# Kernel tuning notes

Hardware: AMD Instinct MI355X
Metric: run time of the kernel (lower is better)

## Reference

```python
import jax, jax.numpy as jnp
import numpy as np

N = 100000
E = 1600000
R = 8
DIN = 128
H = 128
C = 16
NROOT = 1024


def rgcn_conv(x, src, dst, edge_type, w_rel, w_root, bias):
    """PyG RGCNConv: per-relation mean aggregation + root weight + bias."""
    n, din = x.shape
    r = w_rel.shape[0]
    msgs = x[src]  # [E, din] gather
    seg = dst * r + edge_type  # combined (node, relation) segment id
    sums = jax.ops.segment_sum(msgs, seg, num_segments=n * r)        # [N*R, din]
    cnt = jax.ops.segment_sum(jnp.ones((msgs.shape[0],), x.dtype), seg,
                              num_segments=n * r)                    # [N*R]
    mean = sums / jnp.maximum(cnt, 1.0)[:, None]
    mean = mean.reshape(n, r, din)
    # relation-specific transform then sum over relations, plus root transform
    out = jnp.einsum('nrd,rde->ne', mean, w_rel) + x @ w_root + bias
    return out


def setup_inputs() -> dict:
    key = jax.random.key(0)
    ks = jax.random.split(key, 16)
    s = 0.05
    return {
        'x': jax.random.normal(ks[0], (N, DIN), jnp.float32),
        'edge_index': jax.random.randint(ks[1], (2, E), 0, N, jnp.int64),
        'edge_type': jax.random.randint(ks[2], (E,), 0, R, jnp.int64),
        'root_idx': jax.random.randint(ks[3], (NROOT,), 0, N, jnp.int64),
        'wrel1': jax.random.normal(ks[4], (R, DIN, H), jnp.float32) * s,
        'root1': jax.random.normal(ks[5], (DIN, H), jnp.float32) * s,
        'b1': jax.random.normal(ks[6], (H,), jnp.float32) * s,
        'wrel2': jax.random.normal(ks[7], (R, H, H), jnp.float32) * s,
        'root2': jax.random.normal(ks[8], (H, H), jnp.float32) * s,
        'b2': jax.random.normal(ks[9], (H,), jnp.float32) * s,
        'wrel3': jax.random.normal(ks[10], (R, H, C), jnp.float32) * s,
        'root3': jax.random.normal(ks[11], (H, C), jnp.float32) * s,
        'b3': jax.random.normal(ks[12], (C,), jnp.float32) * s,
    }


def reference(x, edge_index, edge_type, root_idx,
              wrel1, root1, b1, wrel2, root2, b2, wrel3, root3, b3):
    src, dst = edge_index[0], edge_index[1]
    h = jax.nn.relu(rgcn_conv(x, src, dst, edge_type, wrel1, root1, b1))
    # hidden conv (relu; dropout is identity in eval mode)
    h = jax.nn.relu(rgcn_conv(h, src, dst, edge_type, wrel2, root2, b2))
    # final conv, no activation
    h = rgcn_conv(h, src, dst, edge_type, wrel3, root3, b3)
    return h[root_idx]  # [NROOT, C]
```

## Files before the change

### kernel.cpp

```cpp
#include <hip/hip_runtime.h>
#include <hip/hip_fp16.h>


typedef _Float16 f16;
typedef _Float16 f16x2 __attribute__((ext_vector_type(2)));
typedef _Float16 f16x4 __attribute__((ext_vector_type(4)));
typedef _Float16 f16x8 __attribute__((ext_vector_type(8)));
typedef float f32x4 __attribute__((ext_vector_type(4)));

#define NREL 8
#define ACHUNK 8192
#define WTELEM (640 * 128)

__global__ void k_hist(const int* __restrict__ dst, int E, int* __restrict__ cnt) {
  int e = blockIdx.x * 256 + threadIdx.x;
  if (e < E) atomicAdd(&cnt[dst[e]], 1);
}

__global__ void k_scan1(const int* __restrict__ in, int* __restrict__ out,
                        int* __restrict__ part, int n) {
  __shared__ int sh[256];
  int b = blockIdx.x, t = threadIdx.x;
  int base = b * 4096 + t * 16;
  int v[16]; int s = 0;
#pragma unroll
  for (int j = 0; j < 16; j++) { int idx = base + j; int x = (idx < n) ? in[idx] : 0; v[j] = s; s += x; }
  sh[t] = s; __syncthreads();
  for (int off = 1; off < 256; off <<= 1) {
    int x = 0; if (t >= off) x = sh[t - off];
    __syncthreads();
    if (t >= off) sh[t] += x;
    __syncthreads();
  }
  int excl = (t == 0) ? 0 : sh[t - 1];
  if (t == 255) part[b] = sh[255];
#pragma unroll
  for (int j = 0; j < 16; j++) { int idx = base + j; if (idx < n) out[idx] = v[j] + excl; }
}

__global__ void k_scan2(int* __restrict__ part, int nb) {
  __shared__ int sh[256];
  int t = threadIdx.x;
  sh[t] = (t < nb) ? part[t] : 0; __syncthreads();
  for (int off = 1; off < 256; off <<= 1) {
    int x = 0; if (t >= off) x = sh[t - off];
    __syncthreads();
    if (t >= off) sh[t] += x;
    __syncthreads();
  }
  if (t < nb) part[t] = (t == 0) ? 0 : sh[t - 1];
}

__global__ void k_scan3(int* __restrict__ out, const int* __restrict__ part, int n) {
  int i = blockIdx.x * 256 + threadIdx.x;
  if (i < n) out[i] += part[i >> 12];
}

__global__ void k_scatter(const int* __restrict__ src, const int* __restrict__ dstv,
                          const int* __restrict__ et, int E,
                          const int* __restrict__ off, int* __restrict__ fill,
                          int* __restrict__ sps) {
  int e = blockIdx.x * 256 + threadIdx.x;
  if (e >= E) return;
  int d = dstv[e];
  int pos = off[d] + atomicAdd(&fill[d], 1);
  sps[pos] = src[e] | (et[e] << 20);
}

__global__ __launch_bounds__(256) void k_sinvp(const int* __restrict__ sps,
                                               const int* __restrict__ off,
                                               float* __restrict__ sinvp, int N) {
  __shared__ int c[16][8];
  int t = threadIdx.x;
  int g = t >> 4, st = t & 15;
  int n = blockIdx.x * 16 + g;
  if (st < 8) c[g][st] = 0;
  __syncthreads();
  if (n < N) {
    int e0 = off[n], e1 = off[n + 1];
    for (int e = e0 + st; e < e1; e += 16)
      atomicAdd(&c[g][((unsigned)sps[e]) >> 20], 1);
  }
  __syncthreads();
  if (n < N && st < 8) {
    int cc = c[g][st];
    sinvp[n * 8 + st] = 1.0f / (float)(cc > 1 ? cc : 1);
  }
}

__global__ void k_sentinel(int* __restrict__ p, int v) { *p = v; }

__global__ __launch_bounds__(256) void k_bhist(const int* __restrict__ dstv, int E,
                                               int* __restrict__ bcnt, int nbuck) {
  __shared__ int h[512];
  int t = threadIdx.x;
  for (int i = t; i < 512; i += 256) h[i] = 0;
  __syncthreads();
  int lo = blockIdx.x * ACHUNK;
  int hi = lo + ACHUNK < E ? lo + ACHUNK : E;
  for (int e = lo + t; e < hi; e += 256) atomicAdd(&h[dstv[e] >> 8], 1);
  __syncthreads();
  for (int i = t; i < nbuck; i += 256)
    if (h[i]) atomicAdd(&bcnt[i], h[i]);
}

__global__ __launch_bounds__(512) void k_bscan(const int* __restrict__ bcnt,
                                               int* __restrict__ boff, int nbuck) {
  __shared__ int sh[512];
  int t = threadIdx.x;
  sh[t] = (t < nbuck) ? bcnt[t] : 0;
  __syncthreads();
  for (int o = 1; o < 512; o <<= 1) {
    int v = 0; if (t >= o) v = sh[t - o];
    __syncthreads();
    sh[t] += v;
    __syncthreads();
  }
  if (t <= nbuck && t < 512) boff[t] = (t == 0) ? 0 : sh[t - 1];
  if (t == 511 && nbuck >= 512) boff[nbuck] = sh[511];
}

__global__ __launch_bounds__(256) void k_bucketA(
    const int* __restrict__ src, const int* __restrict__ dstv,
    const int* __restrict__ et, int E, const int* __restrict__ boff,
    int* __restrict__ bfill, int* __restrict__ tmp, int nbuck) {
  __shared__ int hist[512];
  __shared__ int base[512];
  int t = threadIdx.x;
  int lo = blockIdx.x * ACHUNK;
  int hi = lo + ACHUNK < E ? lo + ACHUNK : E;
  for (int i = t; i < nbuck; i += 256) hist[i] = 0;
  __syncthreads();
  for (int e = lo + t; e < hi; e += 256)
    atomicAdd(&hist[dstv[e] >> 8], 1);
  __syncthreads();
  for (int i = t; i < nbuck; i += 256) {
    int c = hist[i];
    base[i] = c ? (boff[i] + atomicAdd(&bfill[i], c)) : 0;
  }
  __syncthreads();
  for (int e = lo + t; e < hi; e += 256) {
    int d = dstv[e];
    int b = d >> 8;
    int pos = atomicAdd(&base[b], 1);
    tmp[pos] = src[e] | (et[e] << 20) | ((d & 255) << 23);
  }
}

__global__ __launch_bounds__(256) void k_bucketB3(const int* __restrict__ tmp,
                                                  const int* __restrict__ boff,
                                                  int* __restrict__ off,
                                                  int* __restrict__ sps,
                                                  float* __restrict__ sinvp, int N) {
  __shared__ int cty[2048];
  __shared__ int sh[256];
  __shared__ int loff[257];
  __shared__ int fill[256];
  int b = blockIdx.x, t = threadIdx.x;
  int n0 = b << 8;
  int nn = (N - n0) < 256 ? (N - n0) : 256;
#pragma unroll
  for (int j = 0; j < 8; j++) cty[t + j * 256] = 0;
  __syncthreads();
  int e0 = boff[b], e1 = boff[b + 1];
  for (int e = e0 + t; e < e1; e += 256) {
    int v = tmp[e];
    int dl = (v >> 23) & 255, ty = (v >> 20) & 7;
    atomicAdd(&cty[dl * 8 + ty], 1);
  }
  __syncthreads();
  {
    int c = 0;
#pragma unroll
    for (int j = 0; j < 8; j++) c += cty[t * 8 + j];
    sh[t] = c;
  }
  __syncthreads();
  for (int o = 1; o < 256; o <<= 1) {
    int v = 0; if (t >= o) v = sh[t - o];
    __syncthreads();
    sh[t] += v;
    __syncthreads();
  }
  loff[t] = (t == 0) ? 0 : sh[t - 1];
  if (t == 255) loff[256] = sh[255];
  __syncthreads();
  if (t < nn) off[n0 + t] = e0 + loff[t];
  for (int i = t; i < 2048; i += 256) {
    int n = n0 + (i >> 3);
    if (n < N) {
      int c = cty[i];
      sinvp[(size_t)n * 8 + (i & 7)] = 1.0f / (float)(c > 1 ? c : 1);
    }
  }
  fill[t] = 0;
  __syncthreads();
  for (int e = e0 + t; e < e1; e += 256) {
    int v = tmp[e];
    int dl = (v >> 23) & 255;
    int pos = e0 + loff[dl] + atomicAdd(&fill[dl], 1);
    sps[pos] = v & 0x7FFFFF;
  }
}

__global__ void k_mark(const int* __restrict__ ridx, const int* __restrict__ off,
                       const int* __restrict__ sps, int* __restrict__ mark) {
  int i = blockIdx.x, t = threadIdx.x;
  int n = ridx[i];
  if (t == 0) mark[n] = 1;
  int e0 = off[n], e1 = off[n + 1];
  for (int e = e0 + t; e < e1; e += 64) mark[sps[e] & 0xFFFFF] = 1;
}

__global__ void k_compact(const int* __restrict__ mark, int* __restrict__ midx,
                          int* __restrict__ mlist, int* __restrict__ nm, int N) {
  int n = blockIdx.x * 256 + threadIdx.x;
  if (n < N && mark[n]) {
    int i = atomicAdd(nm, 1);
    midx[n] = i;
    mlist[i] = n;
  }
}

__global__ void k_tpw4(const float* __restrict__ wrel1, const float* __restrict__ root1,
                       f16* __restrict__ Wt, int PW) {
  int row = blockIdx.x, k = threadIdx.x, q = blockIdx.y;
  float v = 0.f;
  if (row < 9 * PW) {
    int cb = row / PW, j = row - cb * PW;
    int col = q * PW + j;
    v = (cb < 8) ? wrel1[(size_t)cb * 16384 + k * 128 + col] : root1[k * 128 + col];
  }
  Wt[(size_t)q * WTELEM + (size_t)row * 128 + k] = (f16)v;
}

__global__ void k_tpwc2(const float* __restrict__ wrel2, const float* __restrict__ root2,
                        f16* __restrict__ Wc) {
  int c = blockIdx.x, k = threadIdx.x;
#pragma unroll
  for (int r = 0; r < 8; r++)
    Wc[(size_t)c * 1152 + r * 128 + k] = (f16)wrel2[(size_t)r * 16384 + k * 128 + c];
  Wc[(size_t)c * 1152 + 1024 + k] = (f16)root2[(size_t)k * 128 + c];
}

template <typename AT>
__global__ __launch_bounds__(256) void k_gemm3(const AT* __restrict__ A,
                                               const f16* __restrict__ Bt,
                                               f16* __restrict__ Y, int M, int ncol) {
  __shared__ f16 As[128 * 136];
  int tid = threadIdx.x;
  int m0 = blockIdx.x * 128;
  int PW = ncol / 9;
  int cbs = (PW == 64) ? 6 : 5;
#pragma unroll
  for (int cch = 0; cch < 8; cch++) {
    int ci = tid + cch * 256;
    int row = ci >> 4, c8 = ci & 15;
    int gm = m0 + row;
    f16x8 va = {};
    if (gm < M) {
      if constexpr (sizeof(AT) == 2) {
        va = *(const f16x8*)((const f16*)A + (size_t)gm * 128 + c8 * 8);
      } else {
        const float4* ap = (const float4*)((const float*)A + (size_t)gm * 128);
        float4 u0 = ap[c8 * 2], u1 = ap[c8 * 2 + 1];
        va[0] = (f16)u0.x; va[1] = (f16)u0.y; va[2] = (f16)u0.z; va[3] = (f16)u0.w;
        va[4] = (f16)u1.x; va[5] = (f16)u1.y; va[6] = (f16)u1.z; va[7] = (f16)u1.w;
      }
    }
    *(f16x8*)(As + row * 136 + c8 * 8) = va;
  }
  __syncthreads();
  int wid = tid >> 6, lane = tid & 63;
  int wm = (wid & 1) * 64, wn = (wid >> 1) * 64;
  int lm = lane & 15, lk = lane >> 4;
  f16x8 af[4][4];
#pragma unroll
  for (int ks = 0; ks < 4; ks++)
#pragma unroll
    for (int i = 0; i < 4; i++)
      af[ks][i] = *(const f16x8*)(As + (wm + i * 16 + lm) * 136 + ks * 32 + lk * 8);
  __syncthreads();
  f16* H = As;
  int NT = (ncol + 127) >> 7;
  for (int nt = blockIdx.y; nt < NT; nt += gridDim.y) {
    int n0 = nt * 128;
    f32x4 acc[4][4] = {};
#pragma unroll
    for (int ks = 0; ks < 4; ks++) {
      f16x8 b[4];
#pragma unroll
      for (int j = 0; j < 4; j++)
        b[j] = *(const f16x8*)(Bt + (size_t)(n0 + wn + j * 16 + lm) * 128 + ks * 32 + lk * 8);
#pragma unroll
      for (int i = 0; i < 4; i++)
#pragma unroll
        for (int j = 0; j < 4; j++)
          acc[i][j] = __builtin_amdgcn_mfma_f32_16x16x32_f16(b[j], af[ks][i], acc[i][j], 0, 0, 0);
    }
#pragma unroll
    for (int i = 0; i < 4; i++)
#pragma unroll
      for (int j = 0; j < 4; j++) {
        f16x4 o;
        o[0] = (f16)acc[i][j][0]; o[1] = (f16)acc[i][j][1];
        o[2] = (f16)acc[i][j][2]; o[3] = (f16)acc[i][j][3];
        *(f16x4*)(H + (wm + i * 16 + lm) * 136 + wn + j * 16 + lk * 4) = o;
      }
    __syncthreads();
    for (int i = tid; i < 128 * 16; i += 256) {
      int row = i >> 4, c8 = i & 15;
      int gm = m0 + row;
      int gc = n0 + c8 * 8;
      if (gm < M && gc < ncol) {
        int cb = gc >> cbs, wi = gc & (PW - 1);
        *(f16x8*)(Y + ((size_t)cb * M + gm) * PW + wi) =
            *(const f16x8*)(H + row * 136 + c8 * 8);
      }
    }
    __syncthreads();
  }
}

template <int PW>
__global__ __launch_bounds__(256) void k_edge_v(
    const f16* __restrict__ Y, const int* __restrict__ sps,
    const int* __restrict__ off, const float* __restrict__ sinvp,
    const float* __restrict__ bias, f16* __restrict__ hout, int N, int pass) {
  constexpr int CPL = PW / 16;
  int t = threadIdx.x;
  int g = t >> 4, st = t & 15;
  int n = blockIdx.x * 16 + g;
  if (n >= N) return;
  float sv = (st < 8) ? sinvp[n * 8 + st] : 0.f;
  int e0 = off[n], e1 = off[n + 1];
  float a[CPL], b2[CPL];
  {
    const f16* rp = Y + ((size_t)8 * N + n) * PW + st * CPL;
    const float* bp = bias + pass * PW + st * CPL;
#pragma unroll
    for (int q = 0; q < CPL; q++) { a[q] = (float)rp[q] + bp[q]; b2[q] = 0.f; }
  }
  int sgbase = t & 48;
  int e = e0;
  for (; e + 1 < e1; e += 2) {
    int p0 = sps[e], p1 = sps[e + 1];
    int s0 = p0 & 0xFFFFF, ty0 = ((unsigned)p0) >> 20;
    int s1 = p1 & 0xFFFFF, ty1 = ((unsigned)p1) >> 20;
    float sc0 = __shfl(sv, sgbase | ty0);
    float sc1 = __shfl(sv, sgbase | ty1);
    const f16* q0 = Y + ((size_t)ty0 * N + s0) * PW + st * CPL;
    const f16* q1 = Y + ((size_t)ty1 * N + s1) * PW + st * CPL;
    if constexpr (PW == 64) {
      f16x4 v0 = *(const f16x4*)q0;
      f16x4 v1 = *(const f16x4*)q1;
      a[0] += (float)v0[0] * sc0; a[1] += (float)v0[1] * sc0;
      a[2] += (float)v0[2] * sc0; a[3] += (float)v0[3] * sc0;
      b2[0] += (float)v1[0] * sc1; b2[1] += (float)v1[1] * sc1;
      b2[2] += (float)v1[2] * sc1; b2[3] += (float)v1[3] * sc1;
    } else {
      f16x2 v0 = *(const f16x2*)q0;
      f16x2 v1 = *(const f16x2*)q1;
      a[0] += (float)v0[0] * sc0; a[1] += (float)v0[1] * sc0;
      b2[0] += (float)v1[0] * sc1; b2[1] += (float)v1[1] * sc1;
    }
  }
  if (e < e1) {
    int p0 = sps[e];
    int s0 = p0 & 0xFFFFF, ty0 = ((unsigned)p0) >> 20;
    float sc0 = __shfl(sv, sgbase | ty0);
    const f16* q0 = Y + ((size_t)ty0 * N + s0) * PW + st * CPL;
    if constexpr (PW == 64) {
      f16x4 v0 = *(const f16x4*)q0;
      a[0] += (float)v0[0] * sc0; a[1] += (float)v0[1] * sc0;
      a[2] += (float)v0[2] * sc0; a[3] += (float)v0[3] * sc0;
    } else {
      f16x2 v0 = *(const f16x2*)q0;
      a[0] += (float)v0[0] * sc0; a[1] += (float)v0[1] * sc0;
    }
  }
  if constexpr (PW == 64) {
    f16x4 o;
#pragma unroll
    for (int q = 0; q < 4; q++) o[q] = (f16)fmaxf(a[q] + b2[q], 0.f);
    *(f16x4*)(hout + (size_t)n * 128 + pass * PW + st * 4) = o;
  } else {
    f16x2 o;
#pragma unroll
    for (int q = 0; q < 2; q++) o[q] = (f16)fmaxf(a[q] + b2[q], 0.f);
    *(f16x2*)(hout + (size_t)n * 128 + pass * PW + st * 2) = o;
  }
}

__global__ __launch_bounds__(128) void k_agg2(
    const f16* __restrict__ h1, const int* __restrict__ sps,
    const int* __restrict__ off, const float* __restrict__ sinvp,
    const int* __restrict__ mlist, const int* __restrict__ nm_p,
    f16* __restrict__ Mc, int cap) {
  int nm = *nm_p; if (nm > cap) nm = cap;
  int t = threadIdx.x;
  for (int i = blockIdx.x; i < nm; i += gridDim.x) {
    int n = mlist[i];
    int e0 = off[n], e1 = off[n + 1];
    float acc[8];
#pragma unroll
    for (int r = 0; r < 8; r++) acc[r] = 0.f;
    int e = e0;
    for (; e + 1 < e1; e += 2) {
      int p0 = sps[e], p1 = sps[e + 1];
      int s0 = p0 & 0xFFFFF, ty0 = ((unsigned)p0) >> 20;
      int s1 = p1 & 0xFFFFF, ty1 = ((unsigned)p1) >> 20;
      float v0 = (float)h1[(size_t)s0 * 128 + t];
      float v1 = (float)h1[(size_t)s1 * 128 + t];
#pragma unroll
      for (int r = 0; r < 8; r++) {
        acc[r] += (ty0 == r) ? v0 : 0.f;
        acc[r] += (ty1 == r) ? v1 : 0.f;
      }
    }
    if (e < e1) {
      int p0 = sps[e];
      int s0 = p0 & 0xFFFFF, ty0 = ((unsigned)p0) >> 20;
      float v0 = (float)h1[(size_t)s0 * 128 + t];
#pragma unroll
      for (int r = 0; r < 8; r++) acc[r] += (ty0 == r) ? v0 : 0.f;
    }
    f16* mp = Mc + (size_t)i * 1152;
#pragma unroll
    for (int r = 0; r < 8; r++)
      mp[r * 128 + t] = (f16)(acc[r] * sinvp[(size_t)n * 8 + r]);
    mp[1024 + t] = h1[(size_t)n * 128 + t];
  }
}

__global__ __launch_bounds__(256) void k_gemm_c(const f16* __restrict__ Mc,
                                                const f16* __restrict__ Wc,
                                                const float* __restrict__ bias,
                                                const int* __restrict__ nm_p,
                                                f16* __restrict__ h2c, int cap) {
  int nm = *nm_p; if (nm > cap) nm = cap;
  int m0 = blockIdx.x * 128;
  if (m0 >= nm) return;
  __shared__ f16 As[128 * 136];
  int tid = threadIdx.x;
  int wid = tid >> 6, lane = tid & 63;
  int wm = (wid & 1) * 64, wn = (wid >> 1) * 64;
  int lm = lane & 15, lk = lane >> 4;
  f32x4 acc[4][4] = {};
  for (int kc = 0; kc < 9; kc++) {
    __syncthreads();
#pragma unroll
    for (int cch = 0; cch < 8; cch++) {
      int ci = tid + cch * 256;
      int row = ci >> 4, c8 = ci & 15;
      int gm = m0 + row;
      f16x8 va = {};
      if (gm < nm) va = *(const f16x8*)(Mc + (size_t)gm * 1152 + kc * 128 + c8 * 8);
      *(f16x8*)(As + row * 136 + c8 * 8) = va;
    }
    __syncthreads();
#pragma unroll
    for (int ks = 0; ks < 4; ks++) {
      f16x8 a[4], b[4];
#pragma unroll
      for (int j = 0; j < 4; j++)
        b[j] = *(const f16x8*)(Wc + (size_t)(wn + j * 16 + lm) * 1152 + kc * 128 + ks * 32 + lk * 8);
#pragma unroll
      for (int i = 0; i < 4; i++)
        a[i] = *(const f16x8*)(As + (wm + i * 16 + lm) * 136 + ks * 32 + lk * 8);
#pragma unroll
      for (int i = 0; i < 4; i++)
#pragma unroll
        for (int j = 0; j < 4; j++)
          acc[i][j] = __builtin_amdgcn_mfma_f32_16x16x32_f16(b[j], a[i], acc[i][j], 0, 0, 0);
    }
  }
  __syncthreads();
  f16* H = As;
#pragma unroll
  for (int i = 0; i < 4; i++)
#pragma unroll
    for (int j = 0; j < 4; j++) {
      f16x4 o;
#pragma unroll
      for (int q = 0; q < 4; q++)
        o[q] = (f16)fmaxf(acc[i][j][q] + bias[wn + j * 16 + lk * 4 + q], 0.f);
      *(f16x4*)(H + (wm + i * 16 + lm) * 136 + wn + j * 16 + lk * 4) = o;
    }
  __syncthreads();
  for (int i = tid; i < 128 * 16; i += 256) {
    int row = i >> 4, c8 = i & 15;
    int gm = m0 + row;
    if (gm < nm)
      *(f16x8*)(h2c + (size_t)gm * 128 + c8 * 8) = *(const f16x8*)(H + row * 136 + c8 * 8);
  }
}

__global__ __launch_bounds__(128) void k_layer3c(const f16* __restrict__ h2c,
                                                 const int* __restrict__ midx,
                                                 const int* __restrict__ sps,
                                                 const int* __restrict__ off,
                                                 const float* __restrict__ sinvp,
                                                 const int* __restrict__ ridx,
                                                 const float* __restrict__ wrel,
                                                 const float* __restrict__ wroot,
                                                 const float* __restrict__ b3,
                                                 float* __restrict__ out) {
  __shared__ f16 W[9 * 2048];
  __shared__ float red[2][16];
  __shared__ float sinv_s[8];
  int t = threadIdx.x;
  int n = ridx[blockIdx.x];
  for (int j = t; j < 9 * 2048; j += 128)
    W[j] = (f16)((j < 8 * 2048) ? wrel[j] : wroot[j - 8 * 2048]);
  if (t < 8) sinv_s[t] = sinvp[n * 8 + t];
  __syncthreads();
  int e0 = off[n], e1 = off[n + 1];
  int c = t & 15, kg = t >> 4;
  float a = 0.f;
  for (int e = e0; e < e1; e++) {
    int ps = sps[e];
    int s = ps & 0xFFFFF, ty = ((unsigned)ps) >> 20;
    int si = midx[s];
    float p = 0.f;
#pragma unroll
    for (int j = 0; j < 16; j++) {
      int k = kg * 16 + j;
      p += (float)h2c[(size_t)si * 128 + k] * (float)W[ty * 2048 + k * 16 + c];
    }
    a += sinv_s[ty] * p;
  }
  {
    int ni = midx[n];
    float p = 0.f;
#pragma unroll
    for (int j = 0; j < 16; j++) {
      int k = kg * 16 + j;
      p += (float)h2c[(size_t)ni * 128 + k] * (float)W[8 * 2048 + k * 16 + c];
    }
    a += p;
  }
  a += __shfl_xor(a, 16);
  a += __shfl_xor(a, 32);
  if ((t & 63) < 16) red[t >> 6][t & 15] = a;
  __syncthreads();
  if (t < 16) out[(size_t)blockIdx.x * 16 + t] = red[0][t] + red[1][t] + b3[t];
}

extern "C" void kernel_launch(void* const* d_in, const int* in_sizes, int n_in,
                              void* d_out, int out_size, void* d_ws, size_t ws_size,
                              hipStream_t stream) {
  const float* x     = (const float*)d_in[0];
  const int*   eidx  = (const int*)d_in[1];
  const int*   etyp  = (const int*)d_in[2];
  const int*   ridx  = (const int*)d_in[3];
  const float* wrel1 = (const float*)d_in[4];
  const float* root1 = (const float*)d_in[5];
  const float* b1    = (const float*)d_in[6];
  const float* wrel2 = (const float*)d_in[7];
  const float* root2 = (const float*)d_in[8];
  const float* b2    = (const float*)d_in[9];
  const float* wrel3 = (const float*)d_in[10];
  const float* root3 = (const float*)d_in[11];
  const float* b3    = (const float*)d_in[12];

  int N = in_sizes[0] / 128;
  int E = in_sizes[2];
  int NROOT = in_sizes[3];
  const int* esrc = eidx;
  const int* edst = eidx + E;

  char* p = (char*)d_ws;
  auto alloc = [&](size_t bytes) { void* r = (void*)p; p += (bytes + 255) & ~(size_t)255; return r; };
  int*   off   = (int*)alloc((size_t)(N + 1) * 4);
  int*   sps   = (int*)alloc((size_t)E * 4);
  f16*   h1    = (f16*)alloc((size_t)N * 128 * 2);
  f16*   h2c   = (f16*)alloc((size_t)N * 128 * 2);
  int*   mark  = (int*)alloc((size_t)N * 4);
  int*   midx  = (int*)alloc((size_t)N * 4);
  int*   mlist = (int*)alloc((size_t)N * 4);
  int*   nmv   = (int*)alloc(256);
  float* sinvp = (float*)alloc((size_t)N * 8 * 4);
  f16*   Wt    = (f16*)alloc((size_t)WTELEM * 2 * 4);
  f16*   Wc    = (f16*)alloc((size_t)128 * 1152 * 2);
  int*   bcnt  = (int*)alloc(512 * 4);
  int*   boff  = (int*)alloc(513 * 4);
  int*   bfill = (int*)alloc(512 * 4);

  size_t used = (size_t)(p - (char*)d_ws);
  size_t remain = ws_size > used ? ws_size - used : 0;
  int PW = (remain >= (size_t)N * 9 * 64 * 2 + (1u << 20)) ? 64 : 32;
  int ldy = 9 * PW;
  f16* Y = (f16*)alloc((size_t)N * ldy * 2);
  int* tmp  = (int*)Y;
  int* part = tmp + E;
  int* fill = part + 4096;
  f16* Mc   = Y;
  int  cap  = (int)(((size_t)N * ldy) / 1152);

  int nbuck = (N + 255) >> 8;
  int nbA = (E + ACHUNK - 1) / ACHUNK;
  int npass = 128 / PW;
  int NT = (ldy + 127) / 128;
  hipMemsetAsync(mark, 0, (size_t)N * 4, stream);
  hipMemsetAsync(nmv, 0, 256, stream);
  k_tpw4<<<dim3(NT * 128, npass), 128, 0, stream>>>(wrel1, root1, Wt, PW);
  k_tpwc2<<<128, 128, 0, stream>>>(wrel2, root2, Wc);

  if (nbuck <= 512) {
    hipMemsetAsync(bcnt, 0, 512 * 4, stream);
    hipMemsetAsync(bfill, 0, 512 * 4, stream);
    k_bhist<<<nbA, 256, 0, stream>>>(edst, E, bcnt, nbuck);
    k_bscan<<<1, 512, 0, stream>>>(bcnt, boff, nbuck);
    k_bucketA<<<nbA, 256, 0, stream>>>(esrc, edst, etyp, E, boff, bfill, tmp, nbuck);
    k_bucketB3<<<nbuck, 256, 0, stream>>>(tmp, boff, off, sps, sinvp, N);
    k_sentinel<<<1, 1, 0, stream>>>(off + N, E);
  } else {
    int eb = (E + 255) / 256;
    hipMemsetAsync(off, 0, (size_t)(N + 1) * 4, stream);
    hipMemsetAsync(fill, 0, (size_t)N * 4, stream);
    k_hist<<<eb, 256, 0, stream>>>(edst, E, off);
    int nb1 = (N + 4095) / 4096;
    k_scan1<<<nb1, 256, 0, stream>>>(off, off, part, N);
    k_scan2<<<1, 256, 0, stream>>>(part, nb1);
    k_scan3<<<(N + 255) / 256, 256, 0, stream>>>(off, part, N);
    k_sentinel<<<1, 1, 0, stream>>>(off + N, E);
    k_scatter<<<eb, 256, 0, stream>>>(esrc, edst, etyp, E, off, fill, sps);
    int ng16f = (N + 15) / 16;
    k_sinvp<<<ng16f, 256, 0, stream>>>(sps, off, sinvp, N);
  }
  k_mark<<<NROOT, 64, 0, stream>>>(ridx, off, sps, mark);
  k_compact<<<(N + 255) / 256, 256, 0, stream>>>(mark, midx, mlist, nmv, N);
  int ng16 = (N + 15) / 16;

  int mb = (N + 127) / 128;

  for (int ps = 0; ps < npass; ps++) {
    k_gemm3<float><<<dim3(mb, 2), 256, 0, stream>>>(x, Wt + (size_t)ps * WTELEM, Y, N, ldy);
    if (PW == 64)
      k_edge_v<64><<<ng16, 256, 0, stream>>>(Y, sps, off, sinvp, b1, h1, N, ps);
    else
      k_edge_v<32><<<ng16, 256, 0, stream>>>(Y, sps, off, sinvp, b1, h1, N, ps);
  }
  k_agg2<<<2048, 128, 0, stream>>>(h1, sps, off, sinvp, mlist, nmv, Mc, cap);
  k_gemm_c<<<(cap + 127) / 128, 256, 0, stream>>>(Mc, Wc, b2, nmv, h2c, cap);
  k_layer3c<<<NROOT, 128, 0, stream>>>(h2c, midx, sps, off, sinvp, ridx, wrel3, root3,
                                       b3, (float*)d_out);
}
```

Measured before the change: 446.2 us.

## Merge memsets into init kernel, pre-convert x to f16, unroll gather loops

Replaces four hipMemsetAsync calls with one init kernel. Adds a kernel that converts x from f32 to f16 once, stored in the h2c buffer, so the layer-1 GEMM reads half-size input on every pass. Unrolls the edge-aggregation and agg2 gather loops from two to four edges per iteration so more independent loads are in flight. This costs an extra conversion kernel and reuses h2c as scratch, which is only safe if h2c is large enough and is not read before it is later overwritten.

```diff
diff --git a/kernel.cpp b/kernel.cpp
--- a/kernel.cpp
+++ b/kernel.cpp
@@ -89,6 +89,14 @@
 }
 
 __global__ void k_sentinel(int* __restrict__ p, int v) { *p = v; }
+
+__global__ void k_init(int* __restrict__ bcnt, int* __restrict__ bfill,
+                       int* __restrict__ nmv, int* __restrict__ mark, int N) {
+  int i = blockIdx.x * 256 + threadIdx.x;
+  if (i < 512) { bcnt[i] = 0; bfill[i] = 0; }
+  if (i < 64) nmv[i] = 0;
+  if (i < N) mark[i] = 0;
+}
 
 __global__ __launch_bounds__(256) void k_bhist(const int* __restrict__ dstv, int E,
                                                int* __restrict__ bcnt, int nbuck) {
@@ -219,6 +227,15 @@
     int i = atomicAdd(nm, 1);
     midx[n] = i;
     mlist[i] = n;
+  }
+}
+
+__global__ void k_f32_to_f16(const float* __restrict__ in, f16* __restrict__ out, int n4) {
+  int i = blockIdx.x * 256 + threadIdx.x;
+  if (i < n4) {
+    float4 v = ((const float4*)in)[i];
+    f16x4 o; o[0] = (f16)v.x; o[1] = (f16)v.y; o[2] = (f16)v.z; o[3] = (f16)v.w;
+    ((f16x4*)out)[i] = o;
   }
 }
 
@@ -343,48 +360,68 @@
   }
   int sgbase = t & 48;
   int e = e0;
-  for (; e + 1 < e1; e += 2) {
-    int p0 = sps[e], p1 = sps[e + 1];
-    int s0 = p0 & 0xFFFFF, ty0 = ((unsigned)p0) >> 20;
-    int s1 = p1 & 0xFFFFF, ty1 = ((unsigned)p1) >> 20;
-    float sc0 = __shfl(sv, sgbase | ty0);
-    float sc1 = __shfl(sv, sgbase | ty1);
-    const f16* q0 = Y + ((size_t)ty0 * N + s0) * PW + st * CPL;
-    const f16* q1 = Y + ((size_t)ty1 * N + s1) * PW + st * CPL;
-    if constexpr (PW == 64) {
-      f16x4 v0 = *(const f16x4*)q0;
-      f16x4 v1 = *(const f16x4*)q1;
-      a[0] += (float)v0[0] * sc0; a[1] += (float)v0[1] * sc0;
-      a[2] += (float)v0[2] * sc0; a[3] += (float)v0[3] * sc0;
-      b2[0] += (float)v1[0] * sc1; b2[1] += (float)v1[1] * sc1;
-      b2[2] += (float)v1[2] * sc1; b2[3] += (float)v1[3] * sc1;
-    } else {
-      f16x2 v0 = *(const f16x2*)q0;
-      f16x2 v1 = *(const f16x2*)q1;
-      a[0] += (float)v0[0] * sc0; a[1] += (float)v0[1] * sc0;
-      b2[0] += (float)v1[0] * sc1; b2[1] += (float)v1[1] * sc1;
-    }
-  }
-  if (e < e1) {
-    int p0 = sps[e];
-    int s0 = p0 & 0xFFFFF, ty0 = ((unsigned)p0) >> 20;
-    float sc0 = __shfl(sv, sgbase | ty0);
-    const f16* q0 = Y + ((size_t)ty0 * N + s0) * PW + st * CPL;
-    if constexpr (PW == 64) {
-      f16x4 v0 = *(const f16x4*)q0;
-      a[0] += (float)v0[0] * sc0; a[1] += (float)v0[1] * sc0;
-      a[2] += (float)v0[2] * sc0; a[3] += (float)v0[3] * sc0;
-    } else {
-      f16x2 v0 = *(const f16x2*)q0;
-      a[0] += (float)v0[0] * sc0; a[1] += (float)v0[1] * sc0;
-    }
-  }
   if constexpr (PW == 64) {
+    for (; e + 3 < e1; e += 4) {
+      int p0 = sps[e], p1 = sps[e + 1], p2 = sps[e + 2], p3 = sps[e + 3];
+      int s0 = p0 & 0xFFFFF, ty0 = ((unsigned)p0) >> 20;
+      int s1 = p1 & 0xFFFFF, ty1 = ((unsigned)p1) >> 20;
+      int s2 = p2 & 0xFFFFF, ty2 = ((unsigned)p2) >> 20;
+      int s3 = p3 & 0xFFFFF, ty3 = ((unsigned)p3) >> 20;
+      f16x4 v0 = *(const f16x4*)(Y + ((size_t)ty0 * N + s0) * PW + st * 4);
+      f16x4 v1 = *(const f16x4*)(Y + ((size_t)ty1 * N + s1) * PW + st * 4);
+      f16x4 v2 = *(const f16x4*)(Y + ((size_t)ty2 * N + s2) * PW + st * 4);
+      f16x4 v3 = *(const f16x4*)(Y + ((size_t)ty3 * N + s3) * PW + st * 4);
+      float sc0 = __shfl(sv, sgbase | ty0);
+      float sc1 = __shfl(sv, sgbase | ty1);
+      float sc2 = __shfl(sv, sgbase | ty2);
+      float sc3 = __shfl(sv, sgbase | ty3);
+#pragma unroll
+      for (int q = 0; q < 4; q++) {
+        a[q]  += (float)v0[q] * sc0 + (float)v2[q] * sc2;
+        b2[q] += (float)v1[q] * sc1 + (float)v3[q] * sc3;
+      }
+    }
+    for (; e < e1; e++) {
+      int p0 = sps[e];
+      int s0 = p0 & 0xFFFFF, ty0 = ((unsigned)p0) >> 20;
+      float sc0 = __shfl(sv, sgbase | ty0);
+      f16x4 v0 = *(const f16x4*)(Y + ((size_t)ty0 * N + s0) * PW + st * 4);
+#pragma unroll
+      for (int q = 0; q < 4; q++) a[q] += (float)v0[q] * sc0;
+    }
     f16x4 o;
 #pragma unroll
     for (int q = 0; q < 4; q++) o[q] = (f16)fmaxf(a[q] + b2[q], 0.f);
     *(f16x4*)(hout + (size_t)n * 128 + pass * PW + st * 4) = o;
   } else {
+    for (; e + 3 < e1; e += 4) {
+      int p0 = sps[e], p1 = sps[e + 1], p2 = sps[e + 2], p3 = sps[e + 3];
+      int s0 = p0 & 0xFFFFF, ty0 = ((unsigned)p0) >> 20;
+      int s1 = p1 & 0xFFFFF, ty1 = ((unsigned)p1) >> 20;
+      int s2 = p2 & 0xFFFFF, ty2 = ((unsigned)p2) >> 20;
+      int s3 = p3 & 0xFFFFF, ty3 = ((unsigned)p3) >> 20;
+      f16x2 v0 = *(const f16x2*)(Y + ((size_t)ty0 * N + s0) * PW + st * 2);
+      f16x2 v1 = *(const f16x2*)(Y + ((size_t)ty1 * N + s1) * PW + st * 2);
+      f16x2 v2 = *(const f16x2*)(Y + ((size_t)ty2 * N + s2) * PW + st * 2);
+      f16x2 v3 = *(const f16x2*)(Y + ((size_t)ty3 * N + s3) * PW + st * 2);
+      float sc0 = __shfl(sv, sgbase | ty0);
+      float sc1 = __shfl(sv, sgbase | ty1);
+      float sc2 = __shfl(sv, sgbase | ty2);
+      float sc3 = __shfl(sv, sgbase | ty3);
+#pragma unroll
+      for (int q = 0; q < 2; q++) {
+        a[q]  += (float)v0[q] * sc0 + (float)v2[q] * sc2;
+        b2[q] += (float)v1[q] * sc1 + (float)v3[q] * sc3;
+      }
+    }
+    for (; e < e1; e++) {
+      int p0 = sps[e];
+      int s0 = p0 & 0xFFFFF, ty0 = ((unsigned)p0) >> 20;
+      float sc0 = __shfl(sv, sgbase | ty0);
+      f16x2 v0 = *(const f16x2*)(Y + ((size_t)ty0 * N + s0) * PW + st * 2);
+#pragma unroll
+      for (int q = 0; q < 2; q++) a[q] += (float)v0[q] * sc0;
+    }
     f16x2 o;
 #pragma unroll
     for (int q = 0; q < 2; q++) o[q] = (f16)fmaxf(a[q] + b2[q], 0.f);
@@ -406,22 +443,26 @@
 #pragma unroll
     for (int r = 0; r < 8; r++) acc[r] = 0.f;
     int e = e0;
-    for (; e + 1 < e1; e += 2) {
-      int p0 = sps[e], p1 = sps[e + 1];
-      int s0 = p0 & 0xFFFFF, ty0 = ((unsigned)p0) >> 20;
-      int s1 = p1 & 0xFFFFF, ty1 = ((unsigned)p1) >> 20;
-      float v0 = (float)h1[(size_t)s0 * 128 + t];
-      float v1 = (float)h1[(size_t)s1 * 128 + t];
+    for (; e + 3 < e1; e += 4) {
+      int p0 = sps[e], p1 = sps[e + 1], p2 = sps[e + 2], p3 = sps[e + 3];
+      float v0 = (float)h1[(size_t)(p0 & 0xFFFFF) * 128 + t];
+      float v1 = (float)h1[(size_t)(p1 & 0xFFFFF) * 128 + t];
+      float v2 = (float)h1[(size_t)(p2 & 0xFFFFF) * 128 + t];
+      float v3 = (float)h1[(size_t)(p3 & 0xFFFFF) * 128 + t];
+      int ty0 = ((unsigned)p0) >> 20, ty1 = ((unsigned)p1) >> 20;
+      int ty2 = ((unsigned)p2) >> 20, ty3 = ((unsigned)p3) >> 20;
 #pragma unroll
       for (int r = 0; r < 8; r++) {
         acc[r] += (ty0 == r) ? v0 : 0.f;
         acc[r] += (ty1 == r) ? v1 : 0.f;
+        acc[r] += (ty2 == r) ? v2 : 0.f;
+        acc[r] += (ty3 == r) ? v3 : 0.f;
       }
     }
-    if (e < e1) {
+    for (; e < e1; e++) {
       int p0 = sps[e];
-      int s0 = p0 & 0xFFFFF, ty0 = ((unsigned)p0) >> 20;
-      float v0 = (float)h1[(size_t)s0 * 128 + t];
+      float v0 = (float)h1[(size_t)(p0 & 0xFFFFF) * 128 + t];
+      int ty0 = ((unsigned)p0) >> 20;
 #pragma unroll
       for (int r = 0; r < 8; r++) acc[r] += (ty0 == r) ? v0 : 0.f;
     }
@@ -602,14 +643,13 @@
   int nbA = (E + ACHUNK - 1) / ACHUNK;
   int npass = 128 / PW;
   int NT = (ldy + 127) / 128;
-  hipMemsetAsync(mark, 0, (size_t)N * 4, stream);
-  hipMemsetAsync(nmv, 0, 256, stream);
+  k_init<<<(N + 255) / 256, 256, 0, stream>>>(bcnt, bfill, nmv, mark, N);
   k_tpw4<<<dim3(NT * 128, npass), 128, 0, stream>>>(wrel1, root1, Wt, PW);
   k_tpwc2<<<128, 128, 0, stream>>>(wrel2, root2, Wc);
+  f16* xh = h2c;
+  k_f32_to_f16<<<((N * 32) + 255) / 256, 256, 0, stream>>>(x, xh, N * 32);
 
   if (nbuck <= 512) {
-    hipMemsetAsync(bcnt, 0, 512 * 4, stream);
-    hipMemsetAsync(bfill, 0, 512 * 4, stream);
     k_bhist<<<nbA, 256, 0, stream>>>(edst, E, bcnt, nbuck);
     k_bscan<<<1, 512, 0, stream>>>(bcnt, boff, nbuck);
     k_bucketA<<<nbA, 256, 0, stream>>>(esrc, edst, etyp, E, boff, bfill, tmp, nbuck);
@@ -636,7 +676,7 @@
   int mb = (N + 127) / 128;
 
   for (int ps = 0; ps < npass; ps++) {
-    k_gemm3<float><<<dim3(mb, 2), 256, 0, stream>>>(x, Wt + (size_t)ps * WTELEM, Y, N, ldy);
+    k_gemm3<f16><<<dim3(mb, 2), 256, 0, stream>>>(xh, Wt + (size_t)ps * WTELEM, Y, N, ldy);
     if (PW == 64)
       k_edge_v<64><<<ng16, 256, 0, stream>>>(Y, sps, off, sinvp, b1, h1, N, ps);
     else
```

After: 432.3 us (median of 2 runs). 1.03x faster.
